# Kernel optimization log

Hardware: AMD Instinct MI355X
Metric: run time of the kernel (lower is better)

## Reference

```python
import jax, jax.numpy as jnp
import numpy as np

IN_FEATURES = 4096
OUT_FEATURES = 16384
BATCH = 2
SEQ = 2048


def setup_inputs() -> dict:
    key = jax.random.key(0)
    k_x, k_s, k_sgn, k_b = jax.random.split(key, 4)
    x = jax.random.normal(k_x, (BATCH, SEQ, IN_FEATURES), dtype=jnp.float32)
    # stored: uint8-style inverse-log magnitudes in [1, 255]
    stored = jax.random.randint(k_s, (OUT_FEATURES, IN_FEATURES), 1, 256, dtype=jnp.int32)
    # sign in {0,1}; mapped to {-1,+1} inside reference
    sign = jax.random.randint(k_sgn, (OUT_FEATURES, IN_FEATURES), 0, 2, dtype=jnp.int32)
    # log range matching typical weight magnitudes exp(-8)..exp(0)
    log_min = jnp.full((1,), -8.0, dtype=jnp.float32)
    log_max = jnp.full((1,), 0.0, dtype=jnp.float32)
    bias = jax.random.normal(k_b, (OUT_FEATURES,), dtype=jnp.float32) * 0.02
    return {"x": x, "stored": stored, "sign": sign, "log_min": log_min,
            "log_max": log_max, "bias": bias}


def _dequant_qins(stored, sign, log_min, log_max):
    # reverse inverse mapping: stored in [1,255] -> normalized in [0,1]
    normalized = (255.0 - stored.astype(jnp.float32)) / 254.0
    log_weight = log_min + normalized * (log_max - log_min)
    sign_f = (2 * sign - 1).astype(jnp.float32)  # {0,1} -> {-1,+1}
    return sign_f * jnp.exp(log_weight)  # [out, in] fp32


def reference(x, stored, sign, log_min, log_max, bias):
    lmin = log_min[0]
    lmax = log_max[0]
    w = _dequant_qins(stored, sign, lmin, lmax)  # [O, I]
    # F.linear: y = x @ w.T + bias
    out = jnp.einsum('bsi,oi->bso', x, w) + bias
    return out
```

## Files before the change

### kernel.cpp

```cpp
#include <hip/hip_runtime.h>
#include <stdint.h>

#define M_DIM 4096
#define N_DIM 16384
#define K_DIM 4096
#define BM 256
#define BN 256
#define BK 64
#define NT (K_DIM / BK)

typedef __attribute__((ext_vector_type(8))) __bf16 bf16x8;
typedef __attribute__((ext_vector_type(4))) float f32x4;

__device__ __forceinline__ unsigned short f2bf(float f) {
    uint32_t u = __builtin_bit_cast(uint32_t, f);
    uint32_t r = (u + 0x7FFFu + ((u >> 16) & 1u)) >> 16;
    return (unsigned short)r;
}

union Pack8 { unsigned short h[8]; uint4 v; };

__device__ __forceinline__ void async_copy16(const void* g, void* l) {
    __builtin_amdgcn_global_load_lds((__attribute__((address_space(1))) void*)(g),
                                     (__attribute__((address_space(3))) void*)(l),
                                     16, 0, 0);
}

#define BARRIER() do { asm volatile("" ::: "memory"); \
                       __builtin_amdgcn_s_barrier();  \
                       asm volatile("" ::: "memory"); } while (0)

__global__ __launch_bounds__(256) void cast_x_kernel(const float* __restrict__ x,
                                                     unsigned short* __restrict__ xb,
                                                     int n8) {
    for (int i = blockIdx.x * blockDim.x + threadIdx.x; i < n8;
         i += gridDim.x * blockDim.x) {
        const float4* p = (const float4*)(x + (size_t)i * 8);
        float4 v0 = p[0], v1 = p[1];
        Pack8 o;
        o.h[0] = f2bf(v0.x); o.h[1] = f2bf(v0.y);
        o.h[2] = f2bf(v0.z); o.h[3] = f2bf(v0.w);
        o.h[4] = f2bf(v1.x); o.h[5] = f2bf(v1.y);
        o.h[6] = f2bf(v1.z); o.h[7] = f2bf(v1.w);
        *(uint4*)(xb + (size_t)i * 8) = o.v;
    }
}

__global__ __launch_bounds__(256) void dequant_kernel(const int* __restrict__ stored,
                                                      const int* __restrict__ sign,
                                                      const float* __restrict__ log_min,
                                                      const float* __restrict__ log_max,
                                                      unsigned short* __restrict__ wb,
                                                      int n8) {
    const float lmin = log_min[0];
    const float lrange = log_max[0] - lmin;
    for (int i = blockIdx.x * blockDim.x + threadIdx.x; i < n8;
         i += gridDim.x * blockDim.x) {
        const int4* ps = (const int4*)(stored + (size_t)i * 8);
        const int4* pg = (const int4*)(sign + (size_t)i * 8);
        int4 s0 = ps[0], s1 = ps[1];
        int4 g0 = pg[0], g1 = pg[1];
        int sv[8] = {s0.x, s0.y, s0.z, s0.w, s1.x, s1.y, s1.z, s1.w};
        int gv[8] = {g0.x, g0.y, g0.z, g0.w, g1.x, g1.y, g1.z, g1.w};
        Pack8 o;
#pragma unroll
        for (int j = 0; j < 8; ++j) {
            float nrm = (255.0f - (float)sv[j]) * (1.0f / 254.0f);
            float w = __expf(lmin + nrm * lrange);
            o.h[j] = f2bf(gv[j] ? w : -w);
        }
        *(uint4*)(wb + (size_t)i * 8) = o.v;
    }
}

__global__ __launch_bounds__(512, 2) void gemm_kernel(const unsigned short* __restrict__ A,
                                                      const unsigned short* __restrict__ W,
                                                      const float* __restrict__ bias,
                                                      float* __restrict__ C) {
    extern __shared__ char lds[];
    const int tid  = threadIdx.x;
    const int wave = tid >> 6;
    const int lane = tid & 63;
    const int l15  = lane & 15;
    const int l16  = lane >> 4;
    const int wr   = wave >> 2;
    const int wc   = wave & 3;

    const int bid = blockIdx.x;
    const int wg  = ((bid & 7) << 7) | (bid >> 3);
    const int rowBase = (wg >> 6) * BM;
    const int colBase = (wg & 63) * BN;

    f32x4 acc[8][4] = {};

    auto stage_tile = [&](const unsigned short* g, int rb0, int t, char* buf) {
        const int kb = t * BK;
#pragma unroll
        for (int h = 0; h < 2; ++h) {
            char* hb = buf + h * 16384;
            const int rb = rb0 + h * 128;
#pragma unroll
            for (int sub = 0; sub < 2; ++sub) {
                const int Ld   = (sub * 512 + tid) * 16;
                const int r    = Ld >> 7;
                const int colb = (Ld & 127) ^ ((r & 7) << 4);
                async_copy16(g + (size_t)(rb + r) * K_DIM + kb + (colb >> 1),
                             hb + (sub * 512 + wave * 64) * 16);
            }
        }
    };

    char* pA0 = lds;
    char* pA1 = lds + 32768;
    char* pA2 = lds + 65536;
    char* pB0 = lds + 98304;
    char* pB1 = lds + 131072;

    stage_tile(A, rowBase, 0, pA0);
    stage_tile(W, colBase, 0, pB0);
    stage_tile(A, rowBase, 1, pA1);
    stage_tile(W, colBase, 1, pB1);
    stage_tile(A, rowBase, 2, pA2);
    asm volatile("s_waitcnt vmcnt(12)" ::: "memory");
    BARRIER();

    const int bAoff = wr * 16384;
    const int bBoff = (wc >> 1) * 16384;
    const int brB   = (wc & 1) * 64;

    bf16x8 aF0[4][2], aF1[4][2], bF0[2][2], bF1[2][2];

#pragma unroll
    for (int i = 0; i < 4; ++i)
#pragma unroll
        for (int ks = 0; ks < 2; ++ks) {
            const int r    = i * 16 + l15;
            const int colb = (ks * 64 + l16 * 16) ^ ((r & 7) << 4);
            aF0[i][ks] = *(const bf16x8*)(pA0 + bAoff + (r << 7) + colb);
        }
#pragma unroll
    for (int j = 0; j < 2; ++j)
#pragma unroll
        for (int ks = 0; ks < 2; ++ks) {
            const int r    = brB + j * 16 + l15;
            const int colb = (ks * 64 + l16 * 16) ^ ((r & 7) << 4);
            bF0[j][ks] = *(const bf16x8*)(pB0 + bBoff + (r << 7) + colb);
        }

    for (int t = 0; t < NT; ++t) {
#pragma unroll
        for (int i = 0; i < 4; ++i)
#pragma unroll
            for (int ks = 0; ks < 2; ++ks) {
                const int r    = 64 + i * 16 + l15;
                const int colb = (ks * 64 + l16 * 16) ^ ((r & 7) << 4);
                aF1[i][ks] = *(const bf16x8*)(pA0 + bAoff + (r << 7) + colb);
            }
#pragma unroll
        for (int j = 0; j < 2; ++j)
#pragma unroll
            for (int ks = 0; ks < 2; ++ks) {
                const int r    = brB + 32 + j * 16 + l15;
                const int colb = (ks * 64 + l16 * 16) ^ ((r & 7) << 4);
                bF1[j][ks] = *(const bf16x8*)(pB0 + bBoff + (r << 7) + colb);
            }
        __builtin_amdgcn_s_setprio(1);
#pragma unroll
        for (int i = 0; i < 4; ++i)
#pragma unroll
            for (int j = 0; j < 2; ++j)
#pragma unroll
                for (int ks = 0; ks < 2; ++ks)
                    acc[i][j] = __builtin_amdgcn_mfma_f32_16x16x32_bf16(
                        aF0[i][ks], bF0[j][ks], acc[i][j], 0, 0, 0);
        __builtin_amdgcn_s_setprio(0);

        __builtin_amdgcn_s_setprio(1);
#pragma unroll
        for (int i = 0; i < 4; ++i)
#pragma unroll
            for (int j = 0; j < 2; ++j)
#pragma unroll
                for (int ks = 0; ks < 2; ++ks)
                    acc[i][2 + j] = __builtin_amdgcn_mfma_f32_16x16x32_bf16(
                        aF0[i][ks], bF1[j][ks], acc[i][2 + j], 0, 0, 0);
        __builtin_amdgcn_s_setprio(0);

        __builtin_amdgcn_s_setprio(1);
#pragma unroll
        for (int i = 0; i < 4; ++i)
#pragma unroll
            for (int j = 0; j < 2; ++j)
#pragma unroll
                for (int ks = 0; ks < 2; ++ks)
                    acc[4 + i][j] = __builtin_amdgcn_mfma_f32_16x16x32_bf16(
                        aF1[i][ks], bF0[j][ks], acc[4 + i][j], 0, 0, 0);
        __builtin_amdgcn_s_setprio(0);
        if (t + 2 < NT) asm volatile("s_waitcnt vmcnt(4)" ::: "memory");
        else            asm volatile("s_waitcnt vmcnt(0)" ::: "memory");
        BARRIER();
        __builtin_amdgcn_sched_barrier(0);

        if (t + 2 < NT) stage_tile(W, colBase, t + 2, pB0);
        if (t + 3 < NT) stage_tile(A, rowBase, t + 3, pA0);
        if (t + 1 < NT) {
#pragma unroll
            for (int i = 0; i < 4; ++i)
#pragma unroll
                for (int ks = 0; ks < 2; ++ks) {
                    const int r    = i * 16 + l15;
                    const int colb = (ks * 64 + l16 * 16) ^ ((r & 7) << 4);
                    aF0[i][ks] = *(const bf16x8*)(pA1 + bAoff + (r << 7) + colb);
                }
#pragma unroll
            for (int j = 0; j < 2; ++j)
#pragma unroll
                for (int ks = 0; ks < 2; ++ks) {
                    const int r    = brB + j * 16 + l15;
                    const int colb = (ks * 64 + l16 * 16) ^ ((r & 7) << 4);
                    bF0[j][ks] = *(const bf16x8*)(pB1 + bBoff + (r << 7) + colb);
                }
        }
        __builtin_amdgcn_s_setprio(1);
#pragma unroll
        for (int i = 0; i < 4; ++i)
#pragma unroll
            for (int j = 0; j < 2; ++j)
#pragma unroll
                for (int ks = 0; ks < 2; ++ks)
                    acc[4 + i][2 + j] = __builtin_amdgcn_mfma_f32_16x16x32_bf16(
                        aF1[i][ks], bF1[j][ks], acc[4 + i][2 + j], 0, 0, 0);
        __builtin_amdgcn_s_setprio(0);

        char* ta = pA0; pA0 = pA1; pA1 = pA2; pA2 = ta;
        char* tb = pB0; pB0 = pB1; pB1 = tb;
    }

#pragma unroll
    for (int m = 0; m < 8; ++m) {
        const int grow0 = rowBase + wr * 128 + m * 16 + l16 * 4;
#pragma unroll
        for (int n = 0; n < 4; ++n) {
            const int gcol = colBase + wc * 64 + n * 16 + l15;
            const float bv = bias[gcol];
#pragma unroll
            for (int r4 = 0; r4 < 4; ++r4)
                C[(size_t)(grow0 + r4) * N_DIM + gcol] = acc[m][n][r4] + bv;
        }
    }
}

extern "C" void kernel_launch(void* const* d_in, const int* in_sizes, int n_in,
                              void* d_out, int out_size, void* d_ws, size_t ws_size,
                              hipStream_t stream) {
    const float* x       = (const float*)d_in[0];
    const int*   stored  = (const int*)d_in[1];
    const int*   sign    = (const int*)d_in[2];
    const float* log_min = (const float*)d_in[3];
    const float* log_max = (const float*)d_in[4];
    const float* bias    = (const float*)d_in[5];
    float* out = (float*)d_out;

    unsigned short* Ab = (unsigned short*)d_ws;
    unsigned short* Wb = (unsigned short*)((char*)d_ws +
                          (size_t)M_DIM * K_DIM * sizeof(unsigned short));

    cast_x_kernel<<<2048, 256, 0, stream>>>(x, Ab, (M_DIM * K_DIM) / 8);
    dequant_kernel<<<4096, 256, 0, stream>>>(stored, sign, log_min, log_max, Wb,
                                             (N_DIM * K_DIM) / 8);

    hipFuncSetAttribute((const void*)gemm_kernel,
                        hipFuncAttributeMaxDynamicSharedMemorySize, 163840);
    gemm_kernel<<<dim3((M_DIM / BM) * (N_DIM / BN)), dim3(512), 163840, stream>>>(
        Ab, Wb, bias, out);
}
```

Baseline: 618.9 us.

## Interleave half-tile global-to-LDS loads between MFMA phases with barriers

Global-to-LDS staging of A and W is split into half-tiles, each issued between the four MFMA sub-phases of every K iteration, instead of in one bulk copy after the third phase. Buffer pointers are now computed from t modulo 3 for A and t modulo 2 for W, replacing the rotated pointer variables. Prefetch depth drops to one tile ahead for W and two for A, and each iteration now has about eight workgroup barriers instead of one. The aim is to spread memory traffic evenly across the compute phases, at the cost of more synchronisation stalls and less latency hiding.

New measurement: 625.0 us. About the same (+1.0%).

```diff
diff --git a/kernel.cpp b/kernel.cpp
--- a/kernel.cpp
+++ b/kernel.cpp
@@ -93,77 +93,77 @@
 
     f32x4 acc[8][4] = {};
 
-    auto stage_tile = [&](const unsigned short* g, int rb0, int t, char* buf) {
+    auto stage_half_A = [&](int t, int h) {
         const int kb = t * BK;
-#pragma unroll
-        for (int h = 0; h < 2; ++h) {
-            char* hb = buf + h * 16384;
-            const int rb = rb0 + h * 128;
-#pragma unroll
-            for (int sub = 0; sub < 2; ++sub) {
-                const int Ld   = (sub * 512 + tid) * 16;
-                const int r    = Ld >> 7;
-                const int colb = (Ld & 127) ^ ((r & 7) << 4);
-                async_copy16(g + (size_t)(rb + r) * K_DIM + kb + (colb >> 1),
-                             hb + (sub * 512 + wave * 64) * 16);
-            }
+        char* hb = lds + (t % 3) * 32768 + h * 16384;
+        const int rb = rowBase + h * 128;
+#pragma unroll
+        for (int sub = 0; sub < 2; ++sub) {
+            const int Ld   = (sub * 512 + tid) * 16;
+            const int r    = Ld >> 7;
+            const int colb = (Ld & 127) ^ ((r & 7) << 4);
+            async_copy16(A + (size_t)(rb + r) * K_DIM + kb + (colb >> 1),
+                         hb + (sub * 512 + wave * 64) * 16);
         }
     };
-
-    char* pA0 = lds;
-    char* pA1 = lds + 32768;
-    char* pA2 = lds + 65536;
-    char* pB0 = lds + 98304;
-    char* pB1 = lds + 131072;
-
-    stage_tile(A, rowBase, 0, pA0);
-    stage_tile(W, colBase, 0, pB0);
-    stage_tile(A, rowBase, 1, pA1);
-    stage_tile(W, colBase, 1, pB1);
-    stage_tile(A, rowBase, 2, pA2);
-    asm volatile("s_waitcnt vmcnt(12)" ::: "memory");
+    auto stage_half_B = [&](int t, int h) {
+        const int kb = t * BK;
+        char* hb = lds + 98304 + (t & 1) * 32768 + h * 16384;
+        const int rb = colBase + h * 128;
+#pragma unroll
+        for (int sub = 0; sub < 2; ++sub) {
+            const int Ld   = (sub * 512 + tid) * 16;
+            const int r    = Ld >> 7;
+            const int colb = (Ld & 127) ^ ((r & 7) << 4);
+            async_copy16(W + (size_t)(rb + r) * K_DIM + kb + (colb >> 1),
+                         hb + (sub * 512 + wave * 64) * 16);
+        }
+    };
+
+    stage_half_A(0, 0); stage_half_A(0, 1);
+    stage_half_A(1, 0); stage_half_A(1, 1);
+    stage_half_B(0, 0); stage_half_B(0, 1);
+    asm volatile("s_waitcnt vmcnt(0)" ::: "memory");
     BARRIER();
 
-    const int bAoff = wr * 16384;
-    const int bBoff = (wc >> 1) * 16384;
-    const int brB   = (wc & 1) * 64;
-
+    const int brB = (wc & 1) * 64;
     bf16x8 aF0[4][2], aF1[4][2], bF0[2][2], bF1[2][2];
-
-#pragma unroll
-    for (int i = 0; i < 4; ++i)
-#pragma unroll
-        for (int ks = 0; ks < 2; ++ks) {
-            const int r    = i * 16 + l15;
-            const int colb = (ks * 64 + l16 * 16) ^ ((r & 7) << 4);
-            aF0[i][ks] = *(const bf16x8*)(pA0 + bAoff + (r << 7) + colb);
-        }
-#pragma unroll
-    for (int j = 0; j < 2; ++j)
-#pragma unroll
-        for (int ks = 0; ks < 2; ++ks) {
-            const int r    = brB + j * 16 + l15;
-            const int colb = (ks * 64 + l16 * 16) ^ ((r & 7) << 4);
-            bF0[j][ks] = *(const bf16x8*)(pB0 + bBoff + (r << 7) + colb);
-        }
+    {
+        const char* bA = lds + wr * 16384;
+        const char* bB = lds + 98304 + (wc >> 1) * 16384;
+#pragma unroll
+        for (int i = 0; i < 4; ++i)
+#pragma unroll
+            for (int ks = 0; ks < 2; ++ks) {
+                const int r    = i * 16 + l15;
+                const int colb = (ks * 64 + l16 * 16) ^ ((r & 7) << 4);
+                aF0[i][ks] = *(const bf16x8*)(bA + (r << 7) + colb);
+            }
+#pragma unroll
+        for (int j = 0; j < 2; ++j)
+#pragma unroll
+            for (int ks = 0; ks < 2; ++ks) {
+                const int r    = brB + j * 16 + l15;
+                const int colb = (ks * 64 + l16 * 16) ^ ((r & 7) << 4);
+                bF0[j][ks] = *(const bf16x8*)(bB + (r << 7) + colb);
+            }
+    }
 
     for (int t = 0; t < NT; ++t) {
-#pragma unroll
-        for (int i = 0; i < 4; ++i)
-#pragma unroll
-            for (int ks = 0; ks < 2; ++ks) {
-                const int r    = 64 + i * 16 + l15;
-                const int colb = (ks * 64 + l16 * 16) ^ ((r & 7) << 4);
-                aF1[i][ks] = *(const bf16x8*)(pA0 + bAoff + (r << 7) + colb);
-            }
+        const char* bA = lds + (t % 3) * 32768 + wr * 16384;
+        const char* bB = lds + 98304 + (t & 1) * 32768 + (wc >> 1) * 16384;
+
+        if (t + 1 < NT) stage_half_B(t + 1, 0);
+        BARRIER();
 #pragma unroll
         for (int j = 0; j < 2; ++j)
 #pragma unroll
             for (int ks = 0; ks < 2; ++ks) {
                 const int r    = brB + 32 + j * 16 + l15;
                 const int colb = (ks * 64 + l16 * 16) ^ ((r & 7) << 4);
-                bF1[j][ks] = *(const bf16x8*)(pB0 + bBoff + (r << 7) + colb);
-            }
+                bF1[j][ks] = *(const bf16x8*)(bB + (r << 7) + colb);
+            }
+        __builtin_amdgcn_sched_barrier(0);
         __builtin_amdgcn_s_setprio(1);
 #pragma unroll
         for (int i = 0; i < 4; ++i)
@@ -174,7 +174,19 @@
                     acc[i][j] = __builtin_amdgcn_mfma_f32_16x16x32_bf16(
                         aF0[i][ks], bF0[j][ks], acc[i][j], 0, 0, 0);
         __builtin_amdgcn_s_setprio(0);
-
+        BARRIER();
+
+        if (t + 1 < NT) stage_half_B(t + 1, 1);
+        BARRIER();
+#pragma unroll
+        for (int i = 0; i < 4; ++i)
+#pragma unroll
+            for (int ks = 0; ks < 2; ++ks) {
+                const int r    = 64 + i * 16 + l15;
+                const int colb = (ks * 64 + l16 * 16) ^ ((r & 7) << 4);
+                aF1[i][ks] = *(const bf16x8*)(bA + (r << 7) + colb);
+            }
+        __builtin_amdgcn_sched_barrier(0);
         __builtin_amdgcn_s_setprio(1);
 #pragma unroll
         for (int i = 0; i < 4; ++i)
@@ -185,7 +197,11 @@
                     acc[i][2 + j] = __builtin_amdgcn_mfma_f32_16x16x32_bf16(
                         aF0[i][ks], bF1[j][ks], acc[i][2 + j], 0, 0, 0);
         __builtin_amdgcn_s_setprio(0);
-
+        BARRIER();
+
+        if (t + 2 < NT) stage_half_A(t + 2, 0);
+        BARRIER();
+        __builtin_amdgcn_sched_barrier(0);
         __builtin_amdgcn_s_setprio(1);
 #pragma unroll
         for (int i = 0; i < 4; ++i)
@@ -196,21 +212,22 @@
                     acc[4 + i][j] = __builtin_amdgcn_mfma_f32_16x16x32_bf16(
                         aF1[i][ks], bF0[j][ks], acc[4 + i][j], 0, 0, 0);
         __builtin_amdgcn_s_setprio(0);
-        if (t + 2 < NT) asm volatile("s_waitcnt vmcnt(4)" ::: "memory");
+        BARRIER();
+
+        if (t + 2 < NT) stage_half_A(t + 2, 1);
+        if (t < NT - 2) asm volatile("s_waitcnt vmcnt(4)" ::: "memory");
         else            asm volatile("s_waitcnt vmcnt(0)" ::: "memory");
         BARRIER();
-        __builtin_amdgcn_sched_barrier(0);
-
-        if (t + 2 < NT) stage_tile(W, colBase, t + 2, pB0);
-        if (t + 3 < NT) stage_tile(A, rowBase, t + 3, pA0);
         if (t + 1 < NT) {
+            const char* nA = lds + ((t + 1) % 3) * 32768 + wr * 16384;
+            const char* nB = lds + 98304 + ((t + 1) & 1) * 32768 + (wc >> 1) * 16384;
 #pragma unroll
             for (int i = 0; i < 4; ++i)
 #pragma unroll
                 for (int ks = 0; ks < 2; ++ks) {
                     const int r    = i * 16 + l15;
                     const int colb = (ks * 64 + l16 * 16) ^ ((r & 7) << 4);
-                    aF0[i][ks] = *(const bf16x8*)(pA1 + bAoff + (r << 7) + colb);
+                    aF0[i][ks] = *(const bf16x8*)(nA + (r << 7) + colb);
                 }
 #pragma unroll
             for (int j = 0; j < 2; ++j)
@@ -218,9 +235,10 @@
                 for (int ks = 0; ks < 2; ++ks) {
                     const int r    = brB + j * 16 + l15;
                     const int colb = (ks * 64 + l16 * 16) ^ ((r & 7) << 4);
-                    bF0[j][ks] = *(const bf16x8*)(pB1 + bBoff + (r << 7) + colb);
+                    bF0[j][ks] = *(const bf16x8*)(nB + (r << 7) + colb);
                 }
         }
+        __builtin_amdgcn_sched_barrier(0);
         __builtin_amdgcn_s_setprio(1);
 #pragma unroll
         for (int i = 0; i < 4; ++i)
@@ -231,9 +249,7 @@
                     acc[4 + i][2 + j] = __builtin_amdgcn_mfma_f32_16x16x32_bf16(
                         aF1[i][ks], bF1[j][ks], acc[4 + i][2 + j], 0, 0, 0);
         __builtin_amdgcn_s_setprio(0);
-
-        char* ta = pA0; pA0 = pA1; pA1 = pA2; pA2 = ta;
-        char* tb = pB0; pB0 = pB1; pB1 = tb;
+        BARRIER();
     }
 
 #pragma unroll
```
